# Performance work log

Measured on AMD Instinct MI355X. Metric: run time of the kernel, lower is better.

Reference implementation:

```python
import jax, jax.numpy as jnp
import numpy as np
from functools import partial

L, B, E, H, NL = 512, 16, 768, 12, 12
D = E // H  # head dim = 64
FF = 4 * E
LN_EPS = 1e-5


def gelu_new(x):
    # HF openai-gpt ACT_FNS['gelu'] (tanh approximation)
    c = np.sqrt(2.0 / np.pi).astype(np.float32)
    return 0.5 * x * (1.0 + jnp.tanh(c * (x + 0.044715 * x * x * x)))


def layer_norm(x, g, b):
    mu = jnp.mean(x, axis=-1, keepdims=True)
    var = jnp.mean(jnp.square(x - mu), axis=-1, keepdims=True)
    return (x - mu) * jax.lax.rsqrt(var + LN_EPS) * g + b


def setup_inputs() -> dict:
    key = jax.random.key(0)
    ks = jax.random.split(key, 8)
    s = 0.02
    x = jax.random.normal(ks[0], (L, B, E), dtype=jnp.float32)
    custom_mask = jnp.ones((B, L), dtype=jnp.float32)
    pos_emb = s * jax.random.normal(ks[1], (L, E), dtype=jnp.float32)
    # stacked per-layer params (leading axis = layer)
    params = {
        'c_attn_w': s * jax.random.normal(ks[2], (NL, E, 3 * E), dtype=jnp.float32),
        'c_attn_b': jnp.zeros((NL, 3 * E), dtype=jnp.float32),
        'attn_proj_w': s * jax.random.normal(ks[3], (NL, E, E), dtype=jnp.float32),
        'attn_proj_b': jnp.zeros((NL, E), dtype=jnp.float32),
        'ln1_g': jnp.ones((NL, E), dtype=jnp.float32),
        'ln1_b': jnp.zeros((NL, E), dtype=jnp.float32),
        'c_fc_w': s * jax.random.normal(ks[4], (NL, E, FF), dtype=jnp.float32),
        'c_fc_b': jnp.zeros((NL, FF), dtype=jnp.float32),
        'mlp_proj_w': s * jax.random.normal(ks[5], (NL, FF, E), dtype=jnp.float32),
        'mlp_proj_b': jnp.zeros((NL, E), dtype=jnp.float32),
        'ln2_g': jnp.ones((NL, E), dtype=jnp.float32),
        'ln2_b': jnp.zeros((NL, E), dtype=jnp.float32),
    }
    return {'x': x, 'custom_mask': custom_mask, 'pos_emb': pos_emb, **params}


def _gpt_forward(x, custom_mask, pos_emb, c_attn_w, c_attn_b, attn_proj_w,
                 attn_proj_b, ln1_g, ln1_b, c_fc_w, c_fc_b, mlp_proj_w,
                 mlp_proj_b, ln2_g, ln2_b):
    Lx, Bx, Ex = x.shape
    h = x.transpose(1, 0, 2) + pos_emb[None, :Lx]  # (B, L, E); dropout = eval identity
    # additive padding mask: (1 - m) * finfo.min, broadcast over heads/queries
    add_mask = (1.0 - custom_mask)[:, None, None, :] * jnp.finfo(jnp.float32).min
    causal = jnp.tril(jnp.ones((Lx, Lx), dtype=jnp.float32))  # bias buffer b

    def block(h, p):
        (caw, cab, apw, apb, g1, b1, fw, fb, pw, pb, g2, b2) = p
        qkv = h @ caw + cab                              # (B, L, 3E)
        q, k, v = jnp.split(qkv, 3, axis=-1)
        q = q.reshape(Bx, Lx, H, D).transpose(0, 2, 1, 3)  # (B, H, L, D)
        k = k.reshape(Bx, Lx, H, D).transpose(0, 2, 1, 3)
        v = v.reshape(Bx, Lx, H, D).transpose(0, 2, 1, 3)
        w = jnp.einsum('bhqd,bhkd->bhqk', q, k) / np.float32(np.sqrt(D))
        w = w * causal + (-10000.0) * (1.0 - causal)     # causal bias masking
        w = w + add_mask
        a = jax.nn.softmax(w, axis=-1)
        o = jnp.einsum('bhqk,bhkd->bhqd', a, v)          # (B, H, L, D)
        o = o.transpose(0, 2, 1, 3).reshape(Bx, Lx, Ex)
        a_out = o @ apw + apb
        n = layer_norm(h + a_out, g1, b1)
        m = gelu_new(n @ fw + fb) @ pw + pb
        h2 = layer_norm(n + m, g2, b2)
        return h2, None

    params = (c_attn_w, c_attn_b, attn_proj_w, attn_proj_b, ln1_g, ln1_b,
              c_fc_w, c_fc_b, mlp_proj_w, mlp_proj_b, ln2_g, ln2_b)
    h, _ = jax.lax.scan(block, h, params)
    return h.transpose(1, 0, 2)  # back to (L, B, E)


def reference(x, custom_mask, pos_emb, c_attn_w, c_attn_b, attn_proj_w,
              attn_proj_b, ln1_g, ln1_b, c_fc_w, c_fc_b, mlp_proj_w,
              mlp_proj_b, ln2_g, ln2_b):
    return _gpt_forward(x, custom_mask, pos_emb, c_attn_w, c_attn_b,
                        attn_proj_w, attn_proj_b, ln1_g, ln1_b, c_fc_w,
                        c_fc_b, mlp_proj_w, mlp_proj_b, ln2_g, ln2_b)
```

## Files before the change

kernel.cpp:

```cpp
#include <hip/hip_runtime.h>
#include <cstdint>
#include <cstddef>


#define LSEQ 512
#define NBATCH 16
#define EDIM 768
#define NHEAD 12
#define NLAYER 12

typedef __attribute__((ext_vector_type(8))) short short8;
typedef __attribute__((ext_vector_type(4))) short short4v;
typedef __attribute__((ext_vector_type(4))) float f32x4;

__device__ __forceinline__ short f2bf(float f) {
  union { float f; unsigned u; } x; x.f = f;
  return (short)((x.u + 0x7FFFu + ((x.u >> 16) & 1u)) >> 16);
}
__device__ __forceinline__ float bf2f(short s) {
  union { unsigned u; float f; } x; x.u = ((unsigned)(unsigned short)s) << 16;
  return x.f;
}

__device__ __forceinline__ void gload_lds16(const void* g, void* l) {
  __builtin_amdgcn_global_load_lds(
      (__attribute__((address_space(1))) void*)(void*)g,
      (__attribute__((address_space(3))) void*)l, 16, 0, 0);
}

__global__ __launch_bounds__(256) void wt_transpose(const float* __restrict__ W,
                                                    short* __restrict__ Wt,
                                                    int K, int N) {
  __shared__ float tile[32][33];
  const int n0 = blockIdx.x * 32, k0 = blockIdx.y * 32;
  const size_t lo = (size_t)blockIdx.z * K * N;
  const float* Ws = W + lo;
  short* Wd = Wt + lo;
  const int tx = threadIdx.x & 31, ty = threadIdx.x >> 5;
#pragma unroll
  for (int i = 0; i < 4; ++i)
    tile[ty + i * 8][tx] = Ws[(size_t)(k0 + ty + i * 8) * N + n0 + tx];
  __syncthreads();
#pragma unroll
  for (int i = 0; i < 4; ++i)
    Wd[(size_t)(n0 + ty + i * 8) * K + k0 + tx] = f2bf(tile[tx][ty + i * 8]);
}

__global__ __launch_bounds__(256) void embed_k(const float* __restrict__ x,
                                               const float* __restrict__ pos,
                                               float* __restrict__ h,
                                               short* __restrict__ hbf) {
  const int row = blockIdx.x;
  const int b = row >> 9, lp = row & 511;
  const int t = threadIdx.x;
#pragma unroll
  for (int i = 0; i < 3; ++i) {
    const int e = t + i * 256;
    float v = x[(size_t)(lp * 16 + b) * 768 + e] + pos[(size_t)lp * 768 + e];
    h[(size_t)row * 768 + e] = v;
    hbf[(size_t)row * 768 + e] = f2bf(v);
  }
}

__global__ __launch_bounds__(256) void final_k(const float* __restrict__ h,
                                               float* __restrict__ out) {
  const int row = blockIdx.x;
  const int lp = row >> 4, b = row & 15;
  const int t = threadIdx.x;
#pragma unroll
  for (int i = 0; i < 3; ++i) {
    const int e = t + i * 256;
    out[(size_t)row * 768 + e] = h[(size_t)(b * 512 + lp) * 768 + e];
  }
}

__global__ __launch_bounds__(256) void ln_fused(const float* __restrict__ A,
                                                const short* __restrict__ B,
                                                const float* __restrict__ g,
                                                const float* __restrict__ be,
                                                float* __restrict__ outf,
                                                short* __restrict__ outb) {
  const int row = blockIdx.x * 4 + (threadIdx.x >> 6);
  const int l = threadIdx.x & 63;
  const size_t base = (size_t)row * 768;
  float v[12];
  float s1 = 0.f, s2 = 0.f;
#pragma unroll
  for (int j = 0; j < 3; ++j) {
    const int e = j * 256 + l * 4;
    f32x4 a = *(const f32x4*)&A[base + e];
    short4v b = *(const short4v*)&B[base + e];
#pragma unroll
    for (int q = 0; q < 4; ++q) {
      float x = a[q] + bf2f(b[q]);
      v[j * 4 + q] = x; s1 += x; s2 += x * x;
    }
  }
#pragma unroll
  for (int m = 1; m < 64; m <<= 1) {
    s1 += __shfl_xor(s1, m);
    s2 += __shfl_xor(s2, m);
  }
  const float mu = s1 * (1.f / 768.f);
  const float rs = rsqrtf(s2 * (1.f / 768.f) - mu * mu + 1e-5f);
#pragma unroll
  for (int j = 0; j < 3; ++j) {
    const int e = j * 256 + l * 4;
    f32x4 gv = *(const f32x4*)&g[e];
    f32x4 bv = *(const f32x4*)&be[e];
    f32x4 of; short4v ob;
#pragma unroll
    for (int q = 0; q < 4; ++q) {
      float o = (v[j * 4 + q] - mu) * rs * gv[q] + bv[q];
      of[q] = o; ob[q] = f2bf(o);
    }
    *(f32x4*)&outf[base + e] = of;
    *(short4v*)&outb[base + e] = ob;
  }
}

template <int EPI>
__global__ __launch_bounds__(512, 1) void gemm8(const short* __restrict__ A,
                                                const short* __restrict__ Bt,
                                                const float* __restrict__ bias,
                                                short* __restrict__ C,
                                                int N, int K) {
  __shared__ alignas(16) short Ab[2][256 * 64];
  __shared__ alignas(16) short Bb[2][256 * 64];
  const int t = threadIdx.x;
  const int w = t >> 6, l = t & 63;
  const int wr = w >> 2, wc = w & 3;
  const int l15 = l & 15, lhi = l >> 4;
  const int rowA0 = blockIdx.x * 256;
  const int rowB0 = blockIdx.y * 256;
  const int nk = K >> 6;
  const int sr = l >> 3, sl = l & 7;

  f32x4 acc[8][4];
#pragma unroll
  for (int a = 0; a < 8; ++a)
#pragma unroll
    for (int b = 0; b < 4; ++b) acc[a][b] = (f32x4){0.f, 0.f, 0.f, 0.f};

  auto stageA = [&](int buf, int tile, int half) {
#pragma unroll
    for (int i = 0; i < 2; ++i) {
      const int rb = half * 128 + (i * 8 + w) * 8;
      const int r = rb + sr;
      gload_lds16(A + (size_t)(rowA0 + r) * K + tile * 64 + ((sl ^ (r & 7)) << 3),
                  &Ab[buf][rb * 64]);
    }
  };
  auto stageB = [&](int buf, int tile, int half) {
#pragma unroll
    for (int i = 0; i < 2; ++i) {
      const int rb = half * 128 + (i * 8 + w) * 8;
      const int r = rb + sr;
      gload_lds16(Bt + (size_t)(rowB0 + r) * K + tile * 64 + ((sl ^ (r & 7)) << 3),
                  &Bb[buf][rb * 64]);
    }
  };

  stageA(0, 0, 0); stageA(0, 0, 1);
  stageB(0, 0, 0); stageB(0, 0, 1);
  if (nk > 1) { stageB(1, 1, 0); stageB(1, 1, 1); }
  asm volatile("s_waitcnt vmcnt(4)" ::: "memory");
  __builtin_amdgcn_s_barrier();

  short8 bfr[4][2];
  for (int U = 0; U < nk; ++U) {
    const int cur = U & 1, nxt = cur ^ 1;
#pragma unroll
    for (int p = 0; p < 4; ++p) {
      short8 af[2][2];
#pragma unroll
      for (int rt = 0; rt < 2; ++rt)
#pragma unroll
        for (int kc = 0; kc < 2; ++kc) {
          const int r = wr * 128 + p * 32 + rt * 16 + l15;
          af[rt][kc] = *(const short8*)
              &Ab[cur][r * 64 + ((((kc << 2) | lhi) ^ (r & 7)) << 3)];
        }
      if (p == 0) {
#pragma unroll
        for (int ct = 0; ct < 4; ++ct)
#pragma unroll
          for (int kc = 0; kc < 2; ++kc) {
            const int r = wc * 64 + ct * 16 + l15;
            bfr[ct][kc] = *(const short8*)
                &Bb[cur][r * 64 + ((((kc << 2) | lhi) ^ (r & 7)) << 3)];
          }
      }
      if (p == 0 && U + 1 < nk) stageA(nxt, U + 1, 0);
      if (p == 1 && U + 1 < nk) stageA(nxt, U + 1, 1);
      if (p == 2 && U + 2 < nk) stageB(cur, U + 2, 0);
      if (p == 3 && U + 2 < nk) stageB(cur, U + 2, 1);
      if (p == 3) {
        if (U + 2 < nk) asm volatile("s_waitcnt vmcnt(4)" ::: "memory");
        else            asm volatile("s_waitcnt vmcnt(0)" ::: "memory");
      }
      __builtin_amdgcn_s_barrier();
      asm volatile("s_waitcnt lgkmcnt(0)" ::: "memory");
      __builtin_amdgcn_sched_barrier(0);
      __builtin_amdgcn_s_setprio(1);
#pragma unroll
      for (int rt = 0; rt < 2; ++rt)
#pragma unroll
        for (int ct = 0; ct < 4; ++ct)
#pragma unroll
          for (int kc = 0; kc < 2; ++kc)
            acc[p * 2 + rt][ct] = __builtin_amdgcn_mfma_f32_16x16x32_bf16(
                af[rt][kc], bfr[ct][kc], acc[p * 2 + rt][ct], 0, 0, 0);
      __builtin_amdgcn_s_setprio(0);
      __builtin_amdgcn_s_barrier();
    }
  }

  float bv[4];
#pragma unroll
  for (int ct = 0; ct < 4; ++ct) bv[ct] = bias[rowB0 + wc * 64 + ct * 16 + l15];
#pragma unroll
  for (int rt = 0; rt < 8; ++rt) {
#pragma unroll
    for (int ct = 0; ct < 4; ++ct) {
      const int col = rowB0 + wc * 64 + ct * 16 + l15;
#pragma unroll
      for (int i = 0; i < 4; ++i) {
        const int row = rowA0 + wr * 128 + rt * 16 + lhi * 4 + i;
        float v = acc[rt][ct][i] + bv[ct];
        if constexpr (EPI == 1) {
          C[(size_t)row * N + col] = f2bf(v);
        } else {
          float pz = v * fmaf(0.044715f, v * v, 1.0f);
          float e = __expf(-1.5957691216057308f * pz);
          float r = __builtin_amdgcn_rcpf(1.0f + e);
          C[(size_t)row * N + col] = f2bf(v * r);
        }
      }
    }
  }
}

template <int TN, int EPI>
__global__ __launch_bounds__(256) void gemm_bt(const short* __restrict__ A,
                                               const short* __restrict__ Bt,
                                               const float* __restrict__ bias,
                                               void* __restrict__ C,
                                               int N, int K) {
  constexpr int BK = 64;
  __shared__ alignas(16) short Alds[128 * BK];
  __shared__ alignas(16) short Blds[TN * BK];
  const int t = threadIdx.x;
  const int w = t >> 6, l = t & 63;
  constexpr int WR = (TN == 128) ? 2 : 4;
  constexpr int WC = (TN == 128) ? 2 : 1;
  constexpr int WM = 128 / WR;
  constexpr int MI = WM / 16;
  constexpr int NI = (TN / WC) / 16;
  const int wr = (WC == 2) ? (w >> 1) : w;
  const int wc = (WC == 2) ? (w & 1) : 0;
  const int l15 = l & 15, lhi = l >> 4;
  const int rowA0 = blockIdx.x * 128;
  const int rowB0 = blockIdx.y * TN;
  f32x4 acc[MI][NI];
#pragma unroll
  for (int mi = 0; mi < MI; ++mi)
#pragma unroll
    for (int ni = 0; ni < NI; ++ni) acc[mi][ni] = (f32x4){0.f, 0.f, 0.f, 0.f};

  const int srl = l >> 3;
  const int ss = l & 7;

  for (int kt = 0; kt < K; kt += BK) {
#pragma unroll
    for (int i = 0; i < 4; ++i) {
      const int r = i * 32 + w * 8 + srl;
      gload_lds16(A + (size_t)(rowA0 + r) * K + kt + ((ss ^ (r & 7)) << 3),
                  &Alds[i * 2048 + w * 512]);
    }
#pragma unroll
    for (int i = 0; i < TN / 32; ++i) {
      const int r = i * 32 + w * 8 + srl;
      gload_lds16(Bt + (size_t)(rowB0 + r) * K + kt + ((ss ^ (r & 7)) << 3),
                  &Blds[i * 2048 + w * 512]);
    }
    __syncthreads();
    short8 af[MI][2], bfr[NI][2];
#pragma unroll
    for (int mi = 0; mi < MI; ++mi) {
      const int r = wr * WM + mi * 16 + l15;
#pragma unroll
      for (int kc = 0; kc < 2; ++kc)
        af[mi][kc] = *(const short8*)
            &Alds[r * 64 + ((((kc << 2) | lhi) ^ (r & 7)) << 3)];
    }
#pragma unroll
    for (int ni = 0; ni < NI; ++ni) {
      const int r = wc * 64 + ni * 16 + l15;
#pragma unroll
      for (int kc = 0; kc < 2; ++kc)
        bfr[ni][kc] = *(const short8*)
            &Blds[r * 64 + ((((kc << 2) | lhi) ^ (r & 7)) << 3)];
    }
#pragma unroll
    for (int mi = 0; mi < MI; ++mi)
#pragma unroll
      for (int ni = 0; ni < NI; ++ni)
#pragma unroll
        for (int kc = 0; kc < 2; ++kc)
          acc[mi][ni] = __builtin_amdgcn_mfma_f32_16x16x32_bf16(
              af[mi][kc], bfr[ni][kc], acc[mi][ni], 0, 0, 0);
    __syncthreads();
  }

  float bv[NI];
#pragma unroll
  for (int ni = 0; ni < NI; ++ni) bv[ni] = bias[rowB0 + wc * 64 + ni * 16 + l15];
#pragma unroll
  for (int mi = 0; mi < MI; ++mi) {
#pragma unroll
    for (int ni = 0; ni < NI; ++ni) {
      const int col = rowB0 + wc * 64 + ni * 16 + l15;
#pragma unroll
      for (int i = 0; i < 4; ++i) {
        const int row = rowA0 + wr * WM + mi * 16 + lhi * 4 + i;
        float v = acc[mi][ni][i] + bv[ni];
        if constexpr (EPI == 0) {
          ((float*)C)[(size_t)row * N + col] = v;
        } else {
          ((short*)C)[(size_t)row * N + col] = f2bf(v);
        }
      }
    }
  }
}

__global__ __launch_bounds__(256) void attn_k(const short* __restrict__ qkv,
                                              const float* __restrict__ mask,
                                              short* __restrict__ o) {
  const int qb = blockIdx.x;
  const int hh = blockIdx.y;
  const int b = blockIdx.z;
  const int t = threadIdx.x, w = t >> 6, l = t & 63;
  const int l15 = l & 15, lhi = l >> 4;
  __shared__ alignas(16) short Klds[64 * 64];
  __shared__ alignas(16) short Vlds[64 * 64];
  __shared__ alignas(16) short Plds[4][16 * 72];

  short8 qa[2];
  {
    const size_t base =
        (size_t)(b * LSEQ + qb * 64 + w * 16 + l15) * 2304 + hh * 64;
    qa[0] = *(const short8*)&qkv[base + lhi * 8];
    qa[1] = *(const short8*)&qkv[base + 32 + lhi * 8];
  }
  float mrow[4] = {-1e30f, -1e30f, -1e30f, -1e30f};
  float lrow[4] = {0.f, 0.f, 0.f, 0.f};
  const f32x4 zero4 = {0.f, 0.f, 0.f, 0.f};
  f32x4 oacc[4];
#pragma unroll
  for (int nt = 0; nt < 4; ++nt) oacc[nt] = zero4;

  const int nkt = qb + 1;
  for (int kt = 0; kt < nkt; ++kt) {
    __syncthreads();
    {
      const int kr = t >> 2, cc = (t & 3) * 16;
      const size_t grow = (size_t)(b * LSEQ + kt * 64 + kr) * 2304 + hh * 64;
      short8 k0 = *(const short8*)&qkv[grow + 768 + cc];
      short8 k1 = *(const short8*)&qkv[grow + 768 + cc + 8];
      short8 v0 = *(const short8*)&qkv[grow + 1536 + cc];
      short8 v1 = *(const short8*)&qkv[grow + 1536 + cc + 8];
      const int sw = (kr & 7) << 4;
      *(short8*)((char*)Klds + ((kr * 128 + cc * 2) ^ sw)) = k0;
      *(short8*)((char*)Klds + ((kr * 128 + cc * 2 + 16) ^ sw)) = k1;
#pragma unroll
      for (int e = 0; e < 8; ++e) {
        const int n0 = cc + e, n1 = cc + 8 + e;
        ((short*)Vlds)[((n0 * 128 + kr * 2) ^ ((n0 & 7) << 4)) >> 1] = v0[e];
        ((short*)Vlds)[((n1 * 128 + kr * 2) ^ ((n1 & 7) << 4)) >> 1] = v1[e];
      }
    }
    __syncthreads();

    f32x4 s[4];
#pragma unroll
    for (int jt = 0; jt < 4; ++jt) {
      f32x4 z = zero4;
#pragma unroll
      for (int kc = 0; kc < 2; ++kc) {
        const int rowk = jt * 16 + l15;
        short8 kb = *(const short8*)((char*)Klds +
                     ((rowk * 128 + kc * 64 + lhi * 16) ^ ((rowk & 7) << 4)));
        z = __builtin_amdgcn_mfma_f32_16x16x32_bf16(qa[kc], kb, z, 0, 0, 0);
      }
      s[jt] = z;
    }

    float addm[4];
#pragma unroll
    for (int jt = 0; jt < 4; ++jt)
      addm[jt] = (1.0f - mask[b * LSEQ + kt * 64 + jt * 16 + l15]) *
                 -3.402823466e38f;
#pragma unroll
    for (int jt = 0; jt < 4; ++jt) {
      const int colg = kt * 64 + jt * 16 + l15;
#pragma unroll
      for (int i = 0; i < 4; ++i) {
        const int rowg = qb * 64 + w * 16 + lhi * 4 + i;
        float sv = s[jt][i] * 0.125f;
        if (colg > rowg) sv = -10000.0f;
        s[jt][i] = sv + addm[jt];
      }
    }

    float mnew[4], sc[4];
#pragma unroll
    for (int i = 0; i < 4; ++i) {
      float tm = fmaxf(fmaxf(s[0][i], s[1][i]), fmaxf(s[2][i], s[3][i]));
#pragma unroll
      for (int mm = 1; mm < 16; mm <<= 1) tm = fmaxf(tm, __shfl_xor(tm, mm));
      mnew[i] = fmaxf(mrow[i], tm);
      sc[i] = __expf(mrow[i] - mnew[i]);
      mrow[i] = mnew[i];
    }
#pragma unroll
    for (int i = 0; i < 4; ++i) {
      float ts = 0.f;
#pragma unroll
      for (int jt = 0; jt < 4; ++jt) {
        float p = __expf(s[jt][i] - mnew[i]);
        s[jt][i] = p;
        ts += p;
      }
#pragma unroll
      for (int mm = 1; mm < 16; mm <<= 1) ts += __shfl_xor(ts, mm);
      lrow[i] = lrow[i] * sc[i] + ts;
      oacc[0][i] *= sc[i]; oacc[1][i] *= sc[i];
      oacc[2][i] *= sc[i]; oacc[3][i] *= sc[i];
    }

    short* Pw = &Plds[w][0];
#pragma unroll
    for (int jt = 0; jt < 4; ++jt)
#pragma unroll
      for (int i = 0; i < 4; ++i)
        Pw[(lhi * 4 + i) * 72 + jt * 16 + l15] = f2bf(s[jt][i]);
    __syncthreads();
    short8 pa[2];
#pragma unroll
    for (int kc = 0; kc < 2; ++kc)
      pa[kc] = *(const short8*)&Pw[l15 * 72 + kc * 32 + lhi * 8];

#pragma unroll
    for (int nt = 0; nt < 4; ++nt) {
#pragma unroll
      for (int kc = 0; kc < 2; ++kc) {
        const int rown = nt * 16 + l15;
        short8 vb = *(const short8*)((char*)Vlds +
                     ((rown * 128 + kc * 64 + lhi * 16) ^ ((rown & 7) << 4)));
        oacc[nt] = __builtin_amdgcn_mfma_f32_16x16x32_bf16(pa[kc], vb,
                                                           oacc[nt], 0, 0, 0);
      }
    }
  }

#pragma unroll
  for (int i = 0; i < 4; ++i) {
    const size_t row = (size_t)(b * LSEQ + qb * 64 + w * 16 + lhi * 4 + i);
    const float inv = 1.0f / lrow[i];
#pragma unroll
    for (int nt = 0; nt < 4; ++nt)
      o[row * 768 + hh * 64 + nt * 16 + l15] = f2bf(oacc[nt][i] * inv);
  }
}

extern "C" void kernel_launch(void* const* d_in, const int* in_sizes, int n_in,
                              void* d_out, int out_size, void* d_ws,
                              size_t ws_size, hipStream_t stream) {
  const float* x    = (const float*)d_in[0];
  const float* mask = (const float*)d_in[1];
  const float* pos  = (const float*)d_in[2];
  const float* caw  = (const float*)d_in[3];
  const float* cab  = (const float*)d_in[4];
  const float* apw  = (const float*)d_in[5];
  const float* apb  = (const float*)d_in[6];
  const float* g1   = (const float*)d_in[7];
  const float* b1   = (const float*)d_in[8];
  const float* fw   = (const float*)d_in[9];
  const float* fb   = (const float*)d_in[10];
  const float* pw   = (const float*)d_in[11];
  const float* pb   = (const float*)d_in[12];
  const float* g2   = (const float*)d_in[13];
  const float* b2   = (const float*)d_in[14];

  char* ws = (char*)d_ws;
  size_t off = 0;
  auto alloc = [&](size_t bytes) {
    size_t o = off;
    off += (bytes + 255) & ~(size_t)255;
    return o;
  };
  float* h    = (float*)(ws + alloc(8192ull * 768 * 4));
  short* hbf  = (short*)(ws + alloc(8192ull * 768 * 2));
  float* nrm  = (float*)(ws + alloc(8192ull * 768 * 4));
  short* nbf  = (short*)(ws + alloc(8192ull * 768 * 2));
  short* qkvb = (short*)(ws + alloc(8192ull * 2304 * 2));
  short* obf  = (short*)(ws + alloc(8192ull * 768 * 2));
  short* aout = (short*)(ws + alloc(8192ull * 768 * 2));
  short* gbf  = (short*)(ws + alloc(8192ull * 3072 * 2));
  short* wt_attn = (short*)(ws + alloc(12ull * 768 * 2304 * 2));
  short* wt_proj = (short*)(ws + alloc(12ull * 768 * 768 * 2));
  short* wt_fc   = (short*)(ws + alloc(12ull * 768 * 3072 * 2));
  short* wt_mlp  = (short*)(ws + alloc(12ull * 3072 * 768 * 2));
  (void)ws_size; (void)in_sizes; (void)n_in; (void)out_size;

  wt_transpose<<<dim3(2304 / 32, 768 / 32, 12), 256, 0, stream>>>(caw, wt_attn, 768, 2304);
  wt_transpose<<<dim3(768 / 32, 768 / 32, 12), 256, 0, stream>>>(apw, wt_proj, 768, 768);
  wt_transpose<<<dim3(3072 / 32, 768 / 32, 12), 256, 0, stream>>>(fw, wt_fc, 768, 3072);
  wt_transpose<<<dim3(768 / 32, 3072 / 32, 12), 256, 0, stream>>>(pw, wt_mlp, 3072, 768);

  embed_k<<<8192, 256, 0, stream>>>(x, pos, h, hbf);

  for (int L = 0; L < 12; ++L) {
    gemm8<1><<<dim3(32, 9), 512, 0, stream>>>(
        hbf, wt_attn + (size_t)L * 2304 * 768, cab + (size_t)L * 2304, qkvb, 2304, 768);
    attn_k<<<dim3(8, 12, 16), 256, 0, stream>>>(qkvb, mask, obf);
    gemm_bt<64, 1><<<dim3(64, 12), 256, 0, stream>>>(
        obf, wt_proj + (size_t)L * 768 * 768, apb + (size_t)L * 768, aout, 768, 768);
    ln_fused<<<2048, 256, 0, stream>>>(h, aout, g1 + (size_t)L * 768,
                                       b1 + (size_t)L * 768, nrm, nbf);
    gemm8<2><<<dim3(32, 12), 512, 0, stream>>>(
        nbf, wt_fc + (size_t)L * 768 * 3072, fb + (size_t)L * 3072, gbf, 3072, 768);
    gemm_bt<64, 1><<<dim3(64, 12), 256, 0, stream>>>(
        gbf, wt_mlp + (size_t)L * 3072 * 768, pb + (size_t)L * 768, aout, 768, 3072);
    ln_fused<<<2048, 256, 0, stream>>>(nrm, aout, g2 + (size_t)L * 768,
                                       b2 + (size_t)L * 768, h, hbf);
  }

  final_k<<<8192, 256, 0, stream>>>(h, (float*)d_out);
}
```

Before: 3.550 ms.

## Replace pipelined 256x256 GEMM with simpler single-buffered 128x256 tile kernel

Replaces the double-buffered, hand-scheduled 256x256-tile GEMM used for the QKV and FC projections with a single-buffered 128x256-tile kernel that loads, syncs and computes each K step. Halving the M tile doubles the grid (576/768 blocks instead of 288/384), which gives better coverage of the 256 CUs and fewer accumulators per thread, possibly allowing more than one block per CU. In exchange it drops the explicit load/compute overlap, priority hints and fine-grained waitcnt scheduling, so global-load latency is now exposed at each barrier.

```diff
diff --git a/kernel.cpp b/kernel.cpp
--- a/kernel.cpp
+++ b/kernel.cpp
@@ -120,114 +120,95 @@
 }
 
 template <int EPI>
-__global__ __launch_bounds__(512, 1) void gemm8(const short* __restrict__ A,
-                                                const short* __restrict__ Bt,
-                                                const float* __restrict__ bias,
-                                                short* __restrict__ C,
-                                                int N, int K) {
-  __shared__ alignas(16) short Ab[2][256 * 64];
-  __shared__ alignas(16) short Bb[2][256 * 64];
+__global__ __launch_bounds__(512) void gemm512(const short* __restrict__ A,
+                                               const short* __restrict__ Bt,
+                                               const float* __restrict__ bias,
+                                               short* __restrict__ C,
+                                               int N, int K) {
+  constexpr int BK = 64;
+  __shared__ alignas(16) short Alds[128 * BK];
+  __shared__ alignas(16) short Blds[256 * BK];
   const int t = threadIdx.x;
   const int w = t >> 6, l = t & 63;
   const int wr = w >> 2, wc = w & 3;
   const int l15 = l & 15, lhi = l >> 4;
-  const int rowA0 = blockIdx.x * 256;
+  const int rowA0 = blockIdx.x * 128;
   const int rowB0 = blockIdx.y * 256;
-  const int nk = K >> 6;
-  const int sr = l >> 3, sl = l & 7;
-
-  f32x4 acc[8][4];
-#pragma unroll
-  for (int a = 0; a < 8; ++a)
-#pragma unroll
-    for (int b = 0; b < 4; ++b) acc[a][b] = (f32x4){0.f, 0.f, 0.f, 0.f};
-
-  auto stageA = [&](int buf, int tile, int half) {
+
+  f32x4 acc[4][4];
+#pragma unroll
+  for (int mi = 0; mi < 4; ++mi)
+#pragma unroll
+    for (int ni = 0; ni < 4; ++ni) acc[mi][ni] = (f32x4){0.f, 0.f, 0.f, 0.f};
+
+  const int srl = w * 8 + (l >> 3);
+  const int ss = l & 7;
+
+  const short* aptr[2];
+#pragma unroll
+  for (int i = 0; i < 2; ++i) {
+    const int r = i * 64 + srl;
+    aptr[i] = A + (size_t)(rowA0 + r) * K + ((ss ^ (r & 7)) << 3);
+  }
+  const short* bptr[4];
+#pragma unroll
+  for (int i = 0; i < 4; ++i) {
+    const int r = i * 64 + srl;
+    bptr[i] = Bt + (size_t)(rowB0 + r) * K + ((ss ^ (r & 7)) << 3);
+  }
+
+  for (int kt = 0; kt < K; kt += BK) {
 #pragma unroll
     for (int i = 0; i < 2; ++i) {
-      const int rb = half * 128 + (i * 8 + w) * 8;
-      const int r = rb + sr;
-      gload_lds16(A + (size_t)(rowA0 + r) * K + tile * 64 + ((sl ^ (r & 7)) << 3),
-                  &Ab[buf][rb * 64]);
-    }
-  };
-  auto stageB = [&](int buf, int tile, int half) {
-#pragma unroll
-    for (int i = 0; i < 2; ++i) {
-      const int rb = half * 128 + (i * 8 + w) * 8;
-      const int r = rb + sr;
-      gload_lds16(Bt + (size_t)(rowB0 + r) * K + tile * 64 + ((sl ^ (r & 7)) << 3),
-                  &Bb[buf][rb * 64]);
-    }
-  };
-
-  stageA(0, 0, 0); stageA(0, 0, 1);
-  stageB(0, 0, 0); stageB(0, 0, 1);
-  if (nk > 1) { stageB(1, 1, 0); stageB(1, 1, 1); }
-  asm volatile("s_waitcnt vmcnt(4)" ::: "memory");
-  __builtin_amdgcn_s_barrier();
-
-  short8 bfr[4][2];
-  for (int U = 0; U < nk; ++U) {
-    const int cur = U & 1, nxt = cur ^ 1;
-#pragma unroll
-    for (int p = 0; p < 4; ++p) {
-      short8 af[2][2];
-#pragma unroll
-      for (int rt = 0; rt < 2; ++rt)
-#pragma unroll
-        for (int kc = 0; kc < 2; ++kc) {
-          const int r = wr * 128 + p * 32 + rt * 16 + l15;
-          af[rt][kc] = *(const short8*)
-              &Ab[cur][r * 64 + ((((kc << 2) | lhi) ^ (r & 7)) << 3)];
-        }
-      if (p == 0) {
-#pragma unroll
-        for (int ct = 0; ct < 4; ++ct)
-#pragma unroll
-          for (int kc = 0; kc < 2; ++kc) {
-            const int r = wc * 64 + ct * 16 + l15;
-            bfr[ct][kc] = *(const short8*)
-                &Bb[cur][r * 64 + ((((kc << 2) | lhi) ^ (r & 7)) << 3)];
-          }
-      }
-      if (p == 0 && U + 1 < nk) stageA(nxt, U + 1, 0);
-      if (p == 1 && U + 1 < nk) stageA(nxt, U + 1, 1);
-      if (p == 2 && U + 2 < nk) stageB(cur, U + 2, 0);
-      if (p == 3 && U + 2 < nk) stageB(cur, U + 2, 1);
-      if (p == 3) {
-        if (U + 2 < nk) asm volatile("s_waitcnt vmcnt(4)" ::: "memory");
-        else            asm volatile("s_waitcnt vmcnt(0)" ::: "memory");
-      }
-      __builtin_amdgcn_s_barrier();
-      asm volatile("s_waitcnt lgkmcnt(0)" ::: "memory");
-      __builtin_amdgcn_sched_barrier(0);
-      __builtin_amdgcn_s_setprio(1);
-#pragma unroll
-      for (int rt = 0; rt < 2; ++rt)
-#pragma unroll
-        for (int ct = 0; ct < 4; ++ct)
-#pragma unroll
-          for (int kc = 0; kc < 2; ++kc)
-            acc[p * 2 + rt][ct] = __builtin_amdgcn_mfma_f32_16x16x32_bf16(
-                af[rt][kc], bfr[ct][kc], acc[p * 2 + rt][ct], 0, 0, 0);
-      __builtin_amdgcn_s_setprio(0);
-      __builtin_amdgcn_s_barrier();
-    }
+      gload_lds16(aptr[i], &Alds[(i * 64 + w * 8) * BK]);
+      aptr[i] += BK;
+    }
+#pragma unroll
+    for (int i = 0; i < 4; ++i) {
+      gload_lds16(bptr[i], &Blds[(i * 64 + w * 8) * BK]);
+      bptr[i] += BK;
+    }
+    __syncthreads();
+    short8 af[4][2], bfr[4][2];
+#pragma unroll
+    for (int mi = 0; mi < 4; ++mi) {
+      const int r = wr * 64 + mi * 16 + l15;
+#pragma unroll
+      for (int kc = 0; kc < 2; ++kc)
+        af[mi][kc] = *(const short8*)
+            &Alds[r * BK + ((((kc << 2) | lhi) ^ (r & 7)) << 3)];
+    }
+#pragma unroll
+    for (int ni = 0; ni < 4; ++ni) {
+      const int r = wc * 64 + ni * 16 + l15;
+#pragma unroll
+      for (int kc = 0; kc < 2; ++kc)
+        bfr[ni][kc] = *(const short8*)
+            &Blds[r * BK + ((((kc << 2) | lhi) ^ (r & 7)) << 3)];
+    }
+#pragma unroll
+    for (int mi = 0; mi < 4; ++mi)
+#pragma unroll
+      for (int ni = 0; ni < 4; ++ni)
+#pragma unroll
+        for (int kc = 0; kc < 2; ++kc)
+          acc[mi][ni] = __builtin_amdgcn_mfma_f32_16x16x32_bf16(
+              af[mi][kc], bfr[ni][kc], acc[mi][ni], 0, 0, 0);
+    __syncthreads();
   }
 
   float bv[4];
 #pragma unroll
-  for (int ct = 0; ct < 4; ++ct) bv[ct] = bias[rowB0 + wc * 64 + ct * 16 + l15];
-#pragma unroll
-  for (int rt = 0; rt < 8; ++rt) {
-#pragma unroll
-    for (int ct = 0; ct < 4; ++ct) {
-      const int col = rowB0 + wc * 64 + ct * 16 + l15;
+  for (int ni = 0; ni < 4; ++ni) bv[ni] = bias[rowB0 + wc * 64 + ni * 16 + l15];
+#pragma unroll
+  for (int mi = 0; mi < 4; ++mi) {
+#pragma unroll
+    for (int ni = 0; ni < 4; ++ni) {
+      const int col = rowB0 + wc * 64 + ni * 16 + l15;
 #pragma unroll
       for (int i = 0; i < 4; ++i) {
-        const int row = rowA0 + wr * 128 + rt * 16 + lhi * 4 + i;
-        float v = acc[rt][ct][i] + bv[ct];
+        const int row = rowA0 + wr * 64 + mi * 16 + lhi * 4 + i;
+        float v = acc[mi][ni][i] + bv[ni];
         if constexpr (EPI == 1) {
           C[(size_t)row * N + col] = f2bf(v);
         } else {
@@ -523,14 +504,14 @@
   embed_k<<<8192, 256, 0, stream>>>(x, pos, h, hbf);
 
   for (int L = 0; L < 12; ++L) {
-    gemm8<1><<<dim3(32, 9), 512, 0, stream>>>(
+    gemm512<1><<<dim3(64, 9), 512, 0, stream>>>(
         hbf, wt_attn + (size_t)L * 2304 * 768, cab + (size_t)L * 2304, qkvb, 2304, 768);
     attn_k<<<dim3(8, 12, 16), 256, 0, stream>>>(qkvb, mask, obf);
     gemm_bt<64, 1><<<dim3(64, 12), 256, 0, stream>>>(
         obf, wt_proj + (size_t)L * 768 * 768, apb + (size_t)L * 768, aout, 768, 768);
     ln_fused<<<2048, 256, 0, stream>>>(h, aout, g1 + (size_t)L * 768,
                                        b1 + (size_t)L * 768, nrm, nbf);
-    gemm8<2><<<dim3(32, 12), 512, 0, stream>>>(
+    gemm512<2><<<dim3(64, 12), 512, 0, stream>>>(
         nbf, wt_fc + (size_t)L * 768 * 3072, fb + (size_t)L * 3072, gbf, 3072, 768);
     gemm_bt<64, 1><<<dim3(64, 12), 256, 0, stream>>>(
         gbf, wt_mlp + (size_t)L * 3072 * 768, pb + (size_t)L * 768, aout, 768, 3072);
```

New measurement: 3.364 ms. 5.2% less time.
